# Kernel optimization log

Hardware: AMD Instinct MI355X
Metric: run time of the kernel (lower is better)

Reference implementation:

```python
import jax, jax.numpy as jnp
import numpy as np

N = 8192
D = 512
EPS = 1e-12  # F.normalize default eps


def setup_inputs() -> dict:
    key = jax.random.key(0)
    k1, k2 = jax.random.split(key)
    cur = jax.random.normal(k1, (N, D), dtype=jnp.float32)
    # randn -> mixed-sign entries, so every row of (incidence_m > 0) is unique
    # (the only case where the original `incidence_m += head` shapes agree).
    incidence_m = jax.random.normal(k2, (N, N), dtype=jnp.float32)
    return {"cur": cur, "incidence_m": incidence_m}


def reference(cur, incidence_m):
    # construct_directed: dedup rows of (incidence_m > 0); with all rows unique,
    # each node is its own hyperedge leader and head == mask as float, row order
    # preserved. head is built from python ints in torch, hence non-differentiable.
    mask = incidence_m > 0
    head = jax.lax.stop_gradient(mask.astype(incidence_m.dtype))  # [N, N]
    # F.normalize(head, dim=-1): L2 per row with eps clamp
    head = head / jnp.maximum(
        jnp.sqrt(jnp.sum(head * head, axis=-1, keepdims=True)), EPS
    )
    inc = incidence_m + head                          # [N, N]
    edge_fea = inc @ cur                              # [N, D]
    edge_degree = jnp.sum(inc, axis=-1, keepdims=True)  # [N, 1]
    return edge_fea / edge_degree
```

## Files before the change

### kernel.cpp

```cpp
#include <hip/hip_runtime.h>
#include <stdint.h>


#define NROWS 8192
#define DDIM  512

typedef float f32x4 __attribute__((ext_vector_type(4)));
typedef short s16x8 __attribute__((ext_vector_type(8)));

__device__ __forceinline__ unsigned short f2bf(float f) {
  union { float f; unsigned int u; } c; c.f = f;
  unsigned int u = c.u;
  unsigned int r = u + 0x7FFFu + ((u >> 16) & 1u);
  return (unsigned short)(r >> 16);
}

__global__ __launch_bounds__(256) void bprep_kernel(const float* __restrict__ cur,
                                                    unsigned char* __restrict__ bws) {
  int idx = blockIdx.x * 256 + threadIdx.x;
  int n = idx & 511;
  int kg9 = idx >> 9;
  int kt = kg9 >> 3;
  int kg = kg9 & 7;
  int k0 = kt * 64 + kg * 8;
  union { unsigned short h[8]; uint4 q; } u;
#pragma unroll
  for (int e = 0; e < 8; ++e)
    u.h[e] = f2bf(cur[(size_t)(k0 + e) * DDIM + n]);
  int nt = n >> 8, nn = n & 255;
  size_t off = ((size_t)(nt * 128 + kt) << 15) + ((size_t)kg << 12) + ((size_t)nn << 4);
  *(uint4*)(bws + off) = u.q;
}


#define FENCE() __builtin_amdgcn_sched_barrier(0)
#define BARRIER() __builtin_amdgcn_s_barrier()
#define WAITLGKM() asm volatile("s_waitcnt lgkmcnt(0)" ::: "memory")
#define MFMA_ __builtin_amdgcn_mfma_f32_16x16x32_bf16

__global__ __launch_bounds__(512, 4) void gemm_kernel(const float* __restrict__ inc,
                                                      const unsigned char* __restrict__ bws,
                                                      float* __restrict__ out) {
  __shared__ __align__(16) unsigned char smem[16512];
  unsigned char* const buf0 = smem;
  unsigned char* const buf1 = smem + 8192;

  const int tid = threadIdx.x;
  const int lane = tid & 63;
  const int wv = tid >> 6;
  const int r = lane & 15;
  const int q = lane >> 4;

  const int id = blockIdx.x;
  const int nt = (id & 7) >> 2;
  const int mt = (id >> 3) * 4 + (id & 3);
  const int brow = mt * 32;

  const int sm = tid >> 4;
  const int sp = tid & 15;
  const int kgw = sp >> 1, half = sp & 1;
  const float4* gAr = (const float4*)(inc + (size_t)(brow + sm) * NROWS) + sp;
  const int aWr = (kgw << 9) + ((sm ^ kgw) << 4) + (half << 3);

  int aOff[2][2];
#pragma unroll
  for (int kh = 0; kh < 2; ++kh)
#pragma unroll
    for (int rg = 0; rg < 2; ++rg) {
      int kg = kh * 4 + q;
      int row = rg * 16 + r;
      aOff[kh][rg] = (kg << 9) + ((row ^ kg) << 4);
    }

  const unsigned char* gB = bws + ((size_t)(nt * 128) << 15);
  int bOff[4];
#pragma unroll
  for (int kh = 0; kh < 2; ++kh)
#pragma unroll
    for (int cg = 0; cg < 2; ++cg)
      bOff[kh * 2 + cg] = ((kh * 4 + q) << 12) + ((wv * 32 + cg * 16 + r) << 4);

  f32x4 acc1[2][2], acc2[2][2];
#pragma unroll
  for (int a = 0; a < 2; ++a)
#pragma unroll
    for (int b = 0; b < 2; ++b) {
      acc1[a][b] = (f32x4){0.f, 0.f, 0.f, 0.f};
      acc2[a][b] = (f32x4){0.f, 0.f, 0.f, 0.f};
    }

  double s1 = 0.0;
  int cnt = 0;
  float4 x, y;
  s16x8 bX[4], bY[4];

#define ISSUE_A(d, KT) do { d = gAr[(KT) * 16]; } while (0)

#define LOADB(BS, KT) do {                                                                \
    const unsigned char* _g = gB + ((size_t)(KT) << 15);                                  \
    BS[0] = *(const s16x8*)(_g + bOff[0]);                                                \
    BS[1] = *(const s16x8*)(_g + bOff[1]);                                                \
    BS[2] = *(const s16x8*)(_g + bOff[2]);                                                \
    BS[3] = *(const s16x8*)(_g + bOff[3]);                                                \
  } while (0)

#define XFORM(v, BUF) do {                                                                \
    s1 += (double)v.x + (double)v.y + (double)v.z + (double)v.w;                          \
    cnt += (v.x > 0.f) + (v.y > 0.f) + (v.z > 0.f) + (v.w > 0.f);                         \
    unsigned dlo, dhi;                                                                    \
    asm("v_cvt_pk_bf16_f32 %0, %1, %2" : "=v"(dlo) : "v"(v.x), "v"(v.y));                 \
    asm("v_cvt_pk_bf16_f32 %0, %1, %2" : "=v"(dhi) : "v"(v.z), "v"(v.w));                 \
    unsigned mlo = (v.x > 0.f ? 0x3F80u : 0u) | (v.y > 0.f ? 0x3F800000u : 0u);           \
    unsigned mhi = (v.z > 0.f ? 0x3F80u : 0u) | (v.w > 0.f ? 0x3F800000u : 0u);           \
    *(unsigned long long*)((BUF) + aWr) =                                                 \
        (unsigned long long)dlo | ((unsigned long long)dhi << 32);                        \
    *(unsigned long long*)((BUF) + 4096 + aWr) =                                          \
        (unsigned long long)mlo | ((unsigned long long)mhi << 32);                        \
  } while (0)

#define MFMA_TILE(BUF, BS) do {                                                           \
    _Pragma("unroll")                                                                     \
    for (int kh = 0; kh < 2; ++kh) {                                                      \
      s16x8 af0 = *(const s16x8*)((BUF) + aOff[kh][0]);                                   \
      s16x8 af1 = *(const s16x8*)((BUF) + aOff[kh][1]);                                   \
      s16x8 mf0 = *(const s16x8*)((BUF) + 4096 + aOff[kh][0]);                            \
      s16x8 mf1 = *(const s16x8*)((BUF) + 4096 + aOff[kh][1]);                            \
      __builtin_amdgcn_s_setprio(1);                                                      \
      acc1[0][0] = MFMA_(af0, BS[kh * 2 + 0], acc1[0][0], 0, 0, 0);                       \
      acc2[0][0] = MFMA_(mf0, BS[kh * 2 + 0], acc2[0][0], 0, 0, 0);                       \
      acc1[0][1] = MFMA_(af0, BS[kh * 2 + 1], acc1[0][1], 0, 0, 0);                       \
      acc2[0][1] = MFMA_(mf0, BS[kh * 2 + 1], acc2[0][1], 0, 0, 0);                       \
      acc1[1][0] = MFMA_(af1, BS[kh * 2 + 0], acc1[1][0], 0, 0, 0);                       \
      acc2[1][0] = MFMA_(mf1, BS[kh * 2 + 0], acc2[1][0], 0, 0, 0);                       \
      acc1[1][1] = MFMA_(af1, BS[kh * 2 + 1], acc1[1][1], 0, 0, 0);                       \
      acc2[1][1] = MFMA_(mf1, BS[kh * 2 + 1], acc2[1][1], 0, 0, 0);                       \
      __builtin_amdgcn_s_setprio(0);                                                      \
    }                                                                                     \
  } while (0)

#define SYNC() do { FENCE(); WAITLGKM(); FENCE(); BARRIER(); FENCE(); } while (0)

  ISSUE_A(x, 0);
  LOADB(bX, 0);
  ISSUE_A(y, 1);
  XFORM(x, buf0);
  SYNC();

  for (int kt = 0; kt < 126; kt += 2) {
    ISSUE_A(x, kt + 2);
    LOADB(bY, kt + 1);
    FENCE();
    MFMA_TILE(buf0, bX);
    XFORM(y, buf1);
    SYNC();
    ISSUE_A(y, kt + 3);
    LOADB(bX, kt + 2);
    FENCE();
    MFMA_TILE(buf1, bY);
    XFORM(x, buf0);
    SYNC();
  }

  LOADB(bY, 127);
  FENCE();
  MFMA_TILE(buf0, bX);
  XFORM(y, buf1);
  SYNC();
  MFMA_TILE(buf1, bY);

#pragma unroll
  for (int o = 1; o < 16; o <<= 1) {
    s1 += __shfl_xor(s1, o);
    cnt += __shfl_xor(cnt, o);
  }
  __syncthreads();
  float* const invsS = (float*)buf0;
  float* const rdegS = invsS + 32;
  if (sp == 0) {
    double sq = sqrt((double)cnt);
    invsS[sm] = (cnt > 0) ? (float)(1.0 / sq) : 0.0f;
    rdegS[sm] = (float)(1.0 / (s1 + sq));
  }
  __syncthreads();

#pragma unroll
  for (int rg = 0; rg < 2; ++rg) {
#pragma unroll
    for (int cg = 0; cg < 2; ++cg) {
#pragma unroll
      for (int j = 0; j < 4; ++j) {
        int row = rg * 16 + q * 4 + j;
        out[(size_t)(brow + row) * DDIM + nt * 256 + wv * 32 + cg * 16 + r] =
            (acc1[rg][cg][j] + invsS[row] * acc2[rg][cg][j]) * rdegS[row];
      }
    }
  }
#undef ISSUE_A
#undef LOADB
#undef XFORM
#undef MFMA_TILE
#undef SYNC
}

extern "C" void kernel_launch(void* const* d_in, const int* in_sizes, int n_in,
                              void* d_out, int out_size, void* d_ws, size_t ws_size,
                              hipStream_t stream) {
  const float* cur = (const float*)d_in[0];
  const float* incm = (const float*)d_in[1];
  float* out = (float*)d_out;
  unsigned char* bws = (unsigned char*)d_ws;

  hipLaunchKernelGGL(bprep_kernel, dim3((NROWS * DDIM / 8) / 256), dim3(256), 0, stream,
                     cur, bws);
  hipLaunchKernelGGL(gemm_kernel, dim3(512), dim3(512), 0, stream, incm, bws, out);
}
```

Baseline: 166.9 us.

## Precompute bf16 combined incidence matrix and row degrees in a prep pass

Adds a prep kernel that reads the fp32 incidence matrix once and computes per-row sum and positive count. It writes a swizzled bf16 matrix with the normalized mask already added. The GEMM then streams this half-size operand straight into registers with a single MFMA set, with no LDS staging, barriers or dual accumulators. This trades extra global write and read traffic and a large workspace need for half the MFMA work and removal of the repeated fp32 conversion per N tile. If the workspace is too small it falls back to the old kernel.

```diff
diff --git a/kernel.cpp b/kernel.cpp
--- a/kernel.cpp
+++ b/kernel.cpp
@@ -32,19 +32,84 @@
   *(uint4*)(bws + off) = u.q;
 }
 
+__global__ __launch_bounds__(1024) void prep_kernel(const float* __restrict__ inc,
+                                                    float* __restrict__ rdeg,
+                                                    unsigned char* __restrict__ aprime) {
+  const int b = blockIdx.x;
+  const int tid = threadIdx.x;
+  const int rr = tid >> 8;
+  const int c = tid & 255;
+  const int row = b * 4 + rr;
+
+  const f32x4* p = (const f32x4*)(inc + (size_t)row * NROWS + c * 32);
+  f32x4 f0 = p[0], f1 = p[1], f2 = p[2], f3 = p[3];
+  f32x4 f4 = p[4], f5 = p[5], f6 = p[6], f7 = p[7];
+
+  double s = 0.0;
+  int cnt = 0;
+#define STAT(v) do {                                                                      \
+    s += (double)v[0] + (double)v[1] + (double)v[2] + (double)v[3];                       \
+    cnt += (v[0] > 0.f) + (v[1] > 0.f) + (v[2] > 0.f) + (v[3] > 0.f);                     \
+  } while (0)
+  STAT(f0); STAT(f1); STAT(f2); STAT(f3); STAT(f4); STAT(f5); STAT(f6); STAT(f7);
+#undef STAT
+
+#pragma unroll
+  for (int o = 1; o < 64; o <<= 1) {
+    s += __shfl_xor(s, o);
+    cnt += __shfl_xor(cnt, o);
+  }
+  __shared__ double sws[16];
+  __shared__ int cws[16];
+  __shared__ float invS[4];
+  const int wv = tid >> 6, lane = tid & 63;
+  if (lane == 0) { sws[wv] = s; cws[wv] = cnt; }
+  __syncthreads();
+  if (tid < 4) {
+    double S = sws[tid * 4] + sws[tid * 4 + 1] + sws[tid * 4 + 2] + sws[tid * 4 + 3];
+    int C = cws[tid * 4] + cws[tid * 4 + 1] + cws[tid * 4 + 2] + cws[tid * 4 + 3];
+    double sq = sqrt((double)C);
+    invS[tid] = (C > 0) ? (float)(1.0 / sq) : 0.0f;
+    rdeg[b * 4 + tid] = (float)(1.0 / (S + sq));
+  }
+  __syncthreads();
+  const float invr = invS[rr];
+
+  const int mt = row >> 5, rowIn = row & 31;
+  const int kt = c >> 1;
+  const int kgBase = (c & 1) * 4;
+  unsigned char* chunk = aprime + (((size_t)mt * 128 + kt) << 12);
+#define EMIT(lo, hi, I) do {                                                              \
+    int kg = kgBase + (I);                                                                \
+    float a0 = lo[0] + (lo[0] > 0.f ? invr : 0.f);                                        \
+    float a1 = lo[1] + (lo[1] > 0.f ? invr : 0.f);                                        \
+    float a2 = lo[2] + (lo[2] > 0.f ? invr : 0.f);                                        \
+    float a3 = lo[3] + (lo[3] > 0.f ? invr : 0.f);                                        \
+    float a4 = hi[0] + (hi[0] > 0.f ? invr : 0.f);                                        \
+    float a5 = hi[1] + (hi[1] > 0.f ? invr : 0.f);                                        \
+    float a6 = hi[2] + (hi[2] > 0.f ? invr : 0.f);                                        \
+    float a7 = hi[3] + (hi[3] > 0.f ? invr : 0.f);                                        \
+    uint4 w;                                                                              \
+    asm("v_cvt_pk_bf16_f32 %0, %1, %2" : "=v"(w.x) : "v"(a0), "v"(a1));                   \
+    asm("v_cvt_pk_bf16_f32 %0, %1, %2" : "=v"(w.y) : "v"(a2), "v"(a3));                   \
+    asm("v_cvt_pk_bf16_f32 %0, %1, %2" : "=v"(w.z) : "v"(a4), "v"(a5));                   \
+    asm("v_cvt_pk_bf16_f32 %0, %1, %2" : "=v"(w.w) : "v"(a6), "v"(a7));                   \
+    *(uint4*)(chunk + (kg << 9) + ((rowIn ^ kg) << 4)) = w;                               \
+  } while (0)
+  EMIT(f0, f1, 0);
+  EMIT(f2, f3, 1);
+  EMIT(f4, f5, 2);
+  EMIT(f6, f7, 3);
+#undef EMIT
+}
 
 #define FENCE() __builtin_amdgcn_sched_barrier(0)
-#define BARRIER() __builtin_amdgcn_s_barrier()
-#define WAITLGKM() asm volatile("s_waitcnt lgkmcnt(0)" ::: "memory")
 #define MFMA_ __builtin_amdgcn_mfma_f32_16x16x32_bf16
 
-__global__ __launch_bounds__(512, 4) void gemm_kernel(const float* __restrict__ inc,
-                                                      const unsigned char* __restrict__ bws,
-                                                      float* __restrict__ out) {
-  __shared__ __align__(16) unsigned char smem[16512];
-  unsigned char* const buf0 = smem;
-  unsigned char* const buf1 = smem + 8192;
-
+__global__ __launch_bounds__(512, 4) void gemm_fast(const unsigned char* __restrict__ aprime,
+                                                    const unsigned char* __restrict__ bws,
+                                                    const float* __restrict__ rdeg,
+                                                    float* __restrict__ out) {
   const int tid = threadIdx.x;
   const int lane = tid & 63;
   const int wv = tid >> 6;
@@ -56,6 +121,112 @@
   const int mt = (id >> 3) * 4 + (id & 3);
   const int brow = mt * 32;
 
+  const unsigned char* gA = aprime + ((size_t)mt << 19);
+  const unsigned char* gB = bws + ((size_t)(nt * 128) << 15);
+
+  int aOff[4];
+  int bOff[4];
+#pragma unroll
+  for (int kh = 0; kh < 2; ++kh)
+#pragma unroll
+    for (int g = 0; g < 2; ++g) {
+      int kg = kh * 4 + q;
+      int row = g * 16 + r;
+      aOff[kh * 2 + g] = (kg << 9) + ((row ^ kg) << 4);
+      bOff[kh * 2 + g] = (kg << 12) + ((wv * 32 + g * 16 + r) << 4);
+    }
+
+  f32x4 acc[2][2];
+#pragma unroll
+  for (int a = 0; a < 2; ++a)
+#pragma unroll
+    for (int b = 0; b < 2; ++b)
+      acc[a][b] = (f32x4){0.f, 0.f, 0.f, 0.f};
+
+  s16x8 aX[4], aY[4], bX[4], bY[4];
+
+#define LOADA(S, KT) do {                                                                 \
+    const unsigned char* _g = gA + ((size_t)(KT) << 12);                                  \
+    S[0] = *(const s16x8*)(_g + aOff[0]);                                                 \
+    S[1] = *(const s16x8*)(_g + aOff[1]);                                                 \
+    S[2] = *(const s16x8*)(_g + aOff[2]);                                                 \
+    S[3] = *(const s16x8*)(_g + aOff[3]);                                                 \
+  } while (0)
+
+#define LOADB(S, KT) do {                                                                 \
+    const unsigned char* _g = gB + ((size_t)(KT) << 15);                                  \
+    S[0] = *(const s16x8*)(_g + bOff[0]);                                                 \
+    S[1] = *(const s16x8*)(_g + bOff[1]);                                                 \
+    S[2] = *(const s16x8*)(_g + bOff[2]);                                                 \
+    S[3] = *(const s16x8*)(_g + bOff[3]);                                                 \
+  } while (0)
+
+#define MFMA_TILE(A, B) do {                                                              \
+    __builtin_amdgcn_s_setprio(1);                                                        \
+    _Pragma("unroll")                                                                     \
+    for (int kh = 0; kh < 2; ++kh) {                                                      \
+      acc[0][0] = MFMA_(A[kh * 2 + 0], B[kh * 2 + 0], acc[0][0], 0, 0, 0);                \
+      acc[0][1] = MFMA_(A[kh * 2 + 0], B[kh * 2 + 1], acc[0][1], 0, 0, 0);                \
+      acc[1][0] = MFMA_(A[kh * 2 + 1], B[kh * 2 + 0], acc[1][0], 0, 0, 0);                \
+      acc[1][1] = MFMA_(A[kh * 2 + 1], B[kh * 2 + 1], acc[1][1], 0, 0, 0);                \
+    }                                                                                     \
+    __builtin_amdgcn_s_setprio(0);                                                        \
+  } while (0)
+
+  LOADA(aX, 0);
+  LOADB(bX, 0);
+  for (int kt = 0; kt < 126; kt += 2) {
+    LOADA(aY, kt + 1);
+    LOADB(bY, kt + 1);
+    FENCE();
+    MFMA_TILE(aX, bX);
+    LOADA(aX, kt + 2);
+    LOADB(bX, kt + 2);
+    FENCE();
+    MFMA_TILE(aY, bY);
+  }
+  LOADA(aY, 127);
+  LOADB(bY, 127);
+  FENCE();
+  MFMA_TILE(aX, bX);
+  MFMA_TILE(aY, bY);
+
+#pragma unroll
+  for (int rg = 0; rg < 2; ++rg)
+#pragma unroll
+    for (int cg = 0; cg < 2; ++cg)
+#pragma unroll
+      for (int j = 0; j < 4; ++j) {
+        int row = rg * 16 + q * 4 + j;
+        out[(size_t)(brow + row) * DDIM + nt * 256 + wv * 32 + cg * 16 + r] =
+            acc[rg][cg][j] * rdeg[brow + row];
+      }
+#undef LOADA
+#undef LOADB
+#undef MFMA_TILE
+}
+
+#define BARRIER() __builtin_amdgcn_s_barrier()
+#define WAITLGKM() asm volatile("s_waitcnt lgkmcnt(0)" ::: "memory")
+
+__global__ __launch_bounds__(512, 4) void gemm_dual(const float* __restrict__ inc,
+                                                    const unsigned char* __restrict__ bws,
+                                                    float* __restrict__ out) {
+  __shared__ __align__(16) unsigned char smem[16512];
+  unsigned char* const buf0 = smem;
+  unsigned char* const buf1 = smem + 8192;
+
+  const int tid = threadIdx.x;
+  const int lane = tid & 63;
+  const int wv = tid >> 6;
+  const int r = lane & 15;
+  const int q = lane >> 4;
+
+  const int id = blockIdx.x;
+  const int nt = (id & 7) >> 2;
+  const int mt = (id >> 3) * 4 + (id & 3);
+  const int brow = mt * 32;
+
   const int sm = tid >> 4;
   const int sp = tid & 15;
   const int kgw = sp >> 1, half = sp & 1;
@@ -95,15 +266,13 @@
   s16x8 bX[4], bY[4];
 
 #define ISSUE_A(d, KT) do { d = gAr[(KT) * 16]; } while (0)
-
-#define LOADB(BS, KT) do {                                                                \
+#define LOADB2(BS, KT) do {                                                               \
     const unsigned char* _g = gB + ((size_t)(KT) << 15);                                  \
     BS[0] = *(const s16x8*)(_g + bOff[0]);                                                \
     BS[1] = *(const s16x8*)(_g + bOff[1]);                                                \
     BS[2] = *(const s16x8*)(_g + bOff[2]);                                                \
     BS[3] = *(const s16x8*)(_g + bOff[3]);                                                \
   } while (0)
-
 #define XFORM(v, BUF) do {                                                                \
     s1 += (double)v.x + (double)v.y + (double)v.z + (double)v.w;                          \
     cnt += (v.x > 0.f) + (v.y > 0.f) + (v.z > 0.f) + (v.w > 0.f);                         \
@@ -117,8 +286,7 @@
     *(unsigned long long*)((BUF) + 4096 + aWr) =                                          \
         (unsigned long long)mlo | ((unsigned long long)mhi << 32);                        \
   } while (0)
-
-#define MFMA_TILE(BUF, BS) do {                                                           \
+#define MFMA_TILE2(BUF, BS) do {                                                          \
     _Pragma("unroll")                                                                     \
     for (int kh = 0; kh < 2; ++kh) {                                                      \
       s16x8 af0 = *(const s16x8*)((BUF) + aOff[kh][0]);                                   \
@@ -137,36 +305,33 @@
       __builtin_amdgcn_s_setprio(0);                                                      \
     }                                                                                     \
   } while (0)
-
 #define SYNC() do { FENCE(); WAITLGKM(); FENCE(); BARRIER(); FENCE(); } while (0)
 
   ISSUE_A(x, 0);
-  LOADB(bX, 0);
+  LOADB2(bX, 0);
   ISSUE_A(y, 1);
   XFORM(x, buf0);
   SYNC();
-
   for (int kt = 0; kt < 126; kt += 2) {
     ISSUE_A(x, kt + 2);
-    LOADB(bY, kt + 1);
+    LOADB2(bY, kt + 1);
     FENCE();
-    MFMA_TILE(buf0, bX);
+    MFMA_TILE2(buf0, bX);
     XFORM(y, buf1);
     SYNC();
     ISSUE_A(y, kt + 3);
-    LOADB(bX, kt + 2);
+    LOADB2(bX, kt + 2);
     FENCE();
-    MFMA_TILE(buf1, bY);
+    MFMA_TILE2(buf1, bY);
     XFORM(x, buf0);
     SYNC();
   }
-
-  LOADB(bY, 127);
+  LOADB2(bY, 127);
   FENCE();
-  MFMA_TILE(buf0, bX);
+  MFMA_TILE2(buf0, bX);
   XFORM(y, buf1);
   SYNC();
-  MFMA_TILE(buf1, bY);
+  MFMA_TILE2(buf1, bY);
 
 #pragma unroll
   for (int o = 1; o < 16; o <<= 1) {
@@ -184,21 +349,19 @@
   __syncthreads();
 
 #pragma unroll
-  for (int rg = 0; rg < 2; ++rg) {
-#pragma unroll
-    for (int cg = 0; cg < 2; ++cg) {
+  for (int rg = 0; rg < 2; ++rg)
+#pragma unroll
+    for (int cg = 0; cg < 2; ++cg)
 #pragma unroll
       for (int j = 0; j < 4; ++j) {
         int row = rg * 16 + q * 4 + j;
         out[(size_t)(brow + row) * DDIM + nt * 256 + wv * 32 + cg * 16 + r] =
             (acc1[rg][cg][j] + invsS[row] * acc2[rg][cg][j]) * rdegS[row];
       }
-    }
-  }
 #undef ISSUE_A
-#undef LOADB
+#undef LOADB2
 #undef XFORM
-#undef MFMA_TILE
+#undef MFMA_TILE2
 #undef SYNC
 }
 
@@ -208,9 +371,21 @@
   const float* cur = (const float*)d_in[0];
   const float* incm = (const float*)d_in[1];
   float* out = (float*)d_out;
-  unsigned char* bws = (unsigned char*)d_ws;
+  unsigned char* ws = (unsigned char*)d_ws;
+
+  unsigned char* bws = ws;
+  float* rdeg = (float*)(ws + 8388608);
+  unsigned char* aprime = ws + 8421376;
+  const size_t need = 8421376ull + 134217728ull;
 
   hipLaunchKernelGGL(bprep_kernel, dim3((NROWS * DDIM / 8) / 256), dim3(256), 0, stream,
                      cur, bws);
-  hipLaunchKernelGGL(gemm_kernel, dim3(512), dim3(512), 0, stream, incm, bws, out);
-}
+  if (ws_size >= need) {
+    hipLaunchKernelGGL(prep_kernel, dim3(NROWS / 4), dim3(1024), 0, stream,
+                       incm, rdeg, aprime);
+    hipLaunchKernelGGL(gemm_fast, dim3(512), dim3(512), 0, stream,
+                       aprime, bws, rdeg, out);
+  } else {
+    hipLaunchKernelGGL(gemm_dual, dim3(512), dim3(512), 0, stream, incm, bws, out);
+  }
+}
```

Measured after the change: 278.3 us. 66.7% more time.
